# Optimization experiments

Measured on AMD Instinct MI355X. Metric: run time of the kernel, lower is better.

## Reference

```python
import jax, jax.numpy as jnp
import numpy as np
from jax import lax

V, D = 50000, 300          # vocab, word_embed_dim
C, K, H = 256, 3, 256      # conv out_channels, kernel_size, hidden_size
HLU, AH, NC = 512, 256, 2  # hidden_layer_units, attn_hidden, num_classes
B, QL, AL = 64, 40, 60     # batch, question len, answer len
EPS_COS, EPS_BN = 1e-6, 1e-5


def setup_inputs() -> dict:
    key = jax.random.key(0)
    ks = jax.random.split(key, 16)
    r = lambda k, shp: (0.02 * jax.random.normal(k, shp)).astype(jnp.float32)
    return {
        "question": jax.random.randint(ks[0], (B, QL), 0, V, dtype=jnp.int32),
        "answer": jax.random.randint(ks[1], (B, AL), 0, V, dtype=jnp.int32),
        "ext_feats": jnp.zeros((B, 2), jnp.float32),
        "embedding": r(ks[2], (V, D)),
        # sm_cnn (shared for question and answer)
        "sm_convW": r(ks[3], (K, D, C)), "sm_convb": jnp.zeros((C,), jnp.float32),
        "sm_fcW": r(ks[4], (C, H)), "sm_fcb": jnp.zeros((H,), jnp.float32),
        # context_cnn
        "ctx_convW": r(ks[5], (K, D, C)), "ctx_convb": jnp.zeros((C,), jnp.float32),
        "ctx_fcW": r(ks[6], (C, H)), "ctx_fcb": jnp.zeros((H,), jnp.float32),
        # cnn_attn MLP + cnn_prob
        "attnW": r(ks[7], (H + D, AH)), "attnb": jnp.zeros((AH,), jnp.float32),
        "probW": r(ks[8], (AH, 1)),
        # final_layers: Linear(3H, HLU) + BatchNorm1d
        "W1": r(ks[9], (3 * H, HLU)), "b1": jnp.zeros((HLU,), jnp.float32),
        "gamma": jnp.ones((HLU,), jnp.float32), "beta": jnp.zeros((HLU,), jnp.float32),
        # softmax head
        "W2": r(ks[10], (HLU, NC)), "b2": jnp.zeros((NC,), jnp.float32),
    }


def _simple_cnn(x, convW, convb, fcW, fcb):
    # x: [N, L, D]; full-width Kim-CNN == conv1d over time with D input channels
    y = lax.conv_general_dilated(x, convW, (1,), 'VALID',
                                 dimension_numbers=('NWC', 'WIO', 'NWC'))
    y = jax.nn.relu(y + convb)        # [N, L-K+1, C]
    y = jnp.max(y, axis=1)            # max-pool over time -> [N, C]
    return y @ fcW + fcb              # [N, H]


def reference(question, answer, ext_feats, embedding,
              sm_convW, sm_convb, sm_fcW, sm_fcb,
              ctx_convW, ctx_convb, ctx_fcW, ctx_fcb,
              attnW, attnb, probW, W1, b1, gamma, beta, W2, b2):
    sent1 = embedding[question]                    # [B, QL, D]
    sent2 = embedding[answer]                      # [B, AL, D]

    feature1 = _simple_cnn(sent1, sm_convW, sm_convb, sm_fcW, sm_fcb)   # [B, H]
    feature2 = _simple_cnn(sent2, sm_convW, sm_convb, sm_fcW, sm_fcb)   # [B, H]

    # ---- attn_context (gating_source == 'embed') ----
    nq = jnp.linalg.norm(sent1, axis=-1)           # [B, QL]
    na = jnp.linalg.norm(sent2, axis=-1)           # [B, AL]
    dots = jnp.einsum('bqd,bad->bqa', sent1, sent2)
    cos = dots / jnp.maximum(nq[:, :, None] * na[:, None, :], EPS_COS)  # [B, QL, AL]
    attn_answer = sent2[:, None, :, :] * cos[..., None]                 # [B, QL, AL, D]
    attn_answer = attn_answer.reshape(B * QL, AL, D)

    feat = _simple_cnn(attn_answer, ctx_convW, ctx_convb, ctx_fcW, ctx_fcb)  # [B*QL, H]
    qa_comb = jnp.concatenate([feat, sent1.reshape(-1, D)], axis=1)          # [B*QL, H+D]
    score = (jnp.tanh(qa_comb @ attnW + attnb) @ probW).reshape(B, QL)
    cnn_prob = jax.nn.softmax(score, axis=1)                                 # [B, QL]
    feature3 = jnp.sum(feat.reshape(B, QL, H) * cnn_prob[..., None], axis=1)  # [B, H]

    # ---- final layers ----
    feat_comb = jnp.concatenate([feature1, feature2, feature3], axis=1)  # [B, 3H]
    h = feat_comb @ W1 + b1
    mu = jnp.mean(h, axis=0)
    var = jnp.mean((h - mu) ** 2, axis=0)          # biased, BN training mode
    h = (h - mu) / jnp.sqrt(var + EPS_BN) * gamma + beta
    feat_out = jnp.tanh(h)                          # dropout = identity (p=0)

    preds = jax.nn.log_softmax(feat_out @ W2 + b2, axis=1)
    return preds, feat_out
```

## Files before the change

### kernel.cpp

```cpp
#include <hip/hip_runtime.h>
#include <math.h>

#define Bn 64
#define QLn 40
#define ALn 60
#define Dn 300
#define KS 320
#define NQ 1024
#define NA 1536

typedef _Float16 f16x8 __attribute__((ext_vector_type(8)));
typedef __attribute__((ext_vector_type(4))) float f32x4;

__device__ __forceinline__ short f2h(float f) {
  _Float16 h = (_Float16)f;
  return __builtin_bit_cast(short, h);
}
__device__ __forceinline__ float h2f(short s) {
  return (float)__builtin_bit_cast(_Float16, s);
}
__device__ __forceinline__ float2 h2x2(unsigned int p) {
  union { unsigned int u; _Float16 h[2]; } cv; cv.u = p;
  return make_float2((float)cv.h[0], (float)cv.h[1]);
}

__global__ __launch_bounds__(256) void k_prep(
    const int* __restrict__ qIdx, const int* __restrict__ aIdx,
    const float* __restrict__ emb,
    const float* __restrict__ smW, const float* __restrict__ ctxW,
    const float* __restrict__ attnW, const float* __restrict__ ctxfcW,
    const float* __restrict__ ctxfcb, const float* __restrict__ attnb,
    short* __restrict__ Ae1, short* __restrict__ Ae2,
    float* __restrict__ nq, float* __restrict__ na,
    short* __restrict__ BTall, float* __restrict__ Wcat, float* __restrict__ bvec,
    float* __restrict__ numb, float* __restrict__ denb,
    float* __restrict__ logits, int* __restrict__ done) {
  __shared__ float lds[4160];
  int bid = blockIdx.x, tid = threadIdx.x;
  int w = tid >> 6, lane = tid & 63;
  if (bid < 1600) {
    int row = bid * 4 + w;
    const int* idxp; short* Ae; float* nrm; int r;
    if (row < 2560) { idxp = qIdx; Ae = Ae1; nrm = nq; r = row; }
    else { idxp = aIdx; Ae = Ae2; nrm = na; r = row - 2560; }
    int tok = idxp[r];
    const float4* src = (const float4*)(emb + (size_t)tok * Dn);
    short* d = Ae + (size_t)r * KS;
    float ssq = 0.f;
    for (int i = lane; i < 80; i += 64) {
      float4 v = (i < 75) ? src[i] : make_float4(0.f, 0.f, 0.f, 0.f);
      ssq += v.x * v.x + v.y * v.y + v.z * v.z + v.w * v.w;
      short4 h4;
      h4.x = f2h(v.x); h4.y = f2h(v.y); h4.z = f2h(v.z); h4.w = f2h(v.w);
      *(short4*)&d[i * 4] = h4;
    }
    #pragma unroll
    for (int o = 32; o; o >>= 1) ssq += __shfl_down(ssq, o, 64);
    if (lane == 0) nrm[r] = sqrtf(ssq);
  } else if (bid < 1800) {
    int tb = bid - 1600;
    int kt = tb % 5, nt = tb / 5;
    int n0 = nt * 64;
    const float* src; int cb;
    if (n0 < 768)       { src = smW + (n0 >> 8) * 76800; cb = n0 & 255; }
    else if (n0 < 1024) { src = attnW + 65536;           cb = n0 - 768; }
    else if (n0 < 1792) { int m = n0 - 1024; src = smW + (m >> 8) * 76800; cb = m & 255; }
    else                { int m = n0 - 1792; src = ctxW + (m >> 8) * 76800; cb = m & 255; }
    float* tile = lds;
    int nn = tid & 63;
    #pragma unroll
    for (int it = 0; it < 16; ++it) {
      int kl = it * 4 + w;
      int k = kt * 64 + kl;
      tile[kl * 65 + nn] = (k < 300) ? src[(size_t)k * 256 + cb + nn] : 0.f;
    }
    __syncthreads();
    #pragma unroll
    for (int it = 0; it < 16; ++it) {
      int nloc = it * 4 + w;
      int kl = tid & 63;
      float v = tile[kl * 65 + nloc];
      int n = n0 + nloc, k = kt * 64 + kl;
      BTall[(size_t)n * KS + k] = f2h(v);
    }
  } else if (bid < 2057) {
    int k = bid - 1800;
    float* rowv = lds;
    int j = tid;
    rowv[j] = (k < 256) ? ctxfcW[(size_t)k * 256 + j] : ctxfcb[j];
    __syncthreads();
    float a0 = 0.f, a1 = 0.f, a2 = 0.f, a3 = 0.f;
    for (int m = 0; m < 256; m += 4) {
      a0 += rowv[m]     * attnW[(size_t)m * 256 + j];
      a1 += rowv[m + 1] * attnW[(size_t)(m + 1) * 256 + j];
      a2 += rowv[m + 2] * attnW[(size_t)(m + 2) * 256 + j];
      a3 += rowv[m + 3] * attnW[(size_t)(m + 3) * 256 + j];
    }
    float acc = (a0 + a1) + (a2 + a3);
    if (k < 256) {
      Wcat[(size_t)k * 512 + j] = rowv[j];
      Wcat[(size_t)k * 512 + 256 + j] = acc;
    } else {
      bvec[j] = ctxfcb[j];
      bvec[256 + j] = acc + attnb[j];
    }
  } else {
    for (int i = tid; i < Bn * 256; i += 256) numb[i] = 0.f;
    if (tid < Bn) denb[tid] = 0.f;
    if (tid < 2 * Bn) logits[tid] = 0.f;
    if (tid == 0) *done = 0;
  }
}

__device__ __forceinline__ void gl2lds16(const short* g, short* l) {
  __builtin_amdgcn_global_load_lds(
      (const __attribute__((address_space(1))) unsigned int*)g,
      (__attribute__((address_space(3))) unsigned int*)l, 16, 0, 0);
}

__global__ __launch_bounds__(256) void k_mega(
    const short* __restrict__ Ae1, const short* __restrict__ Ae2,
    const short* __restrict__ BTall, short* __restrict__ ZQh, short* __restrict__ ZAh,
    const float* __restrict__ nq, const float* __restrict__ na,
    float* __restrict__ cosb) {
  __shared__ __align__(16) short As[128 * 32];
  __shared__ __align__(16) short Bs[128 * 32];
  int tid = threadIdx.x;
  int wid = tid >> 6, lane = tid & 63;
  int l15 = lane & 15, l4 = lane >> 4;
  int bid = blockIdx.x;
  int lin = (bid & 7) * 73 + (bid >> 3);

  if (lin < 520) {
    const short *A, *BT; short* C; int bx, by, ldc;
    if (lin < 160) {
      int chunk = lin >> 4, ww = lin & 15;
      by = ww >> 1; bx = chunk * 2 + (ww & 1);
      A = Ae1; BT = BTall; C = ZQh; ldc = NQ;
    } else {
      int l2 = lin - 160;
      int chunk = l2 / 24, ww = l2 % 24;
      by = ww >> 1; bx = chunk * 2 + (ww & 1);
      A = Ae2; BT = BTall + (size_t)1024 * KS; C = ZAh; ldc = NA;
    }
    int rowBase = bx * 128, colBase = by * 128;
    int mw = wid * 32;

    f32x4 acc[2][8];
    #pragma unroll
    for (int i = 0; i < 2; ++i)
      #pragma unroll
      for (int j = 0; j < 8; ++j) acc[i][j] = (f32x4){0.f, 0.f, 0.f, 0.f};

    int rowA0 = mw + l15, rowA1 = mw + 16 + l15;
    int sA0 = (l4 ^ ((rowA0 >> 1) & 3)) << 3;
    int sA1 = (l4 ^ ((rowA1 >> 1) & 3)) << 3;

    #pragma unroll 1
    for (int ks = 0; ks < 10; ++ks) {
      int k0 = ks * 32;
      #pragma unroll
      for (int j = 0; j < 2; ++j) {
        int idx = tid + j * 256;
        int r = idx >> 2, s = idx & 3;
        int sl = s ^ ((r >> 1) & 3);
        int chunkStart = j * 256 + wid * 64;
        gl2lds16(A + (size_t)(rowBase + r) * KS + k0 + (sl << 3), &As[chunkStart * 8]);
        gl2lds16(BT + (size_t)(colBase + r) * KS + k0 + (sl << 3), &Bs[chunkStart * 8]);
      }
      __syncthreads();
      f16x8 a0 = *reinterpret_cast<const f16x8*>(&As[rowA0 * 32 + sA0]);
      f16x8 a1 = *reinterpret_cast<const f16x8*>(&As[rowA1 * 32 + sA1]);
      #pragma unroll
      for (int nj = 0; nj < 8; ++nj) {
        int rb = nj * 16 + l15;
        f16x8 bf = *reinterpret_cast<const f16x8*>(&Bs[rb * 32 + ((l4 ^ ((rb >> 1) & 3)) << 3)]);
        acc[0][nj] = __builtin_amdgcn_mfma_f32_16x16x32_f16(a0, bf, acc[0][nj], 0, 0, 0);
        acc[1][nj] = __builtin_amdgcn_mfma_f32_16x16x32_f16(a1, bf, acc[1][nj], 0, 0, 0);
      }
      __syncthreads();
    }
    #pragma unroll
    for (int mi = 0; mi < 2; ++mi) {
      int row0 = rowBase + mw + mi * 16 + l4 * 4;
      #pragma unroll
      for (int nj = 0; nj < 8; ++nj) {
        int col = colBase + nj * 16 + l15;
        #pragma unroll
        for (int r = 0; r < 4; ++r)
          C[(size_t)(row0 + r) * ldc + col] = f2h(acc[mi][nj][r]);
      }
    }
  } else {
    int b = lin - 520;
    int rowBase = b * 40, colBase = b * 60;
    f32x4 cacc[4];
    #pragma unroll
    for (int nj = 0; nj < 4; ++nj) cacc[nj] = (f32x4){0.f, 0.f, 0.f, 0.f};
    int rowA = (wid << 4) + l15;
    int sA = (l4 ^ ((rowA >> 1) & 3)) << 3;

    #pragma unroll 1
    for (int ks = 0; ks < 10; ++ks) {
      int k0 = ks * 32;
      int r = tid >> 2, s = tid & 3;
      int sl = s ^ ((r >> 1) & 3);
      int chunkStart = wid * 64;
      int gr = rowBase + r; if (gr > 2559) gr = 2559;
      int gc = colBase + r; if (gc > 3839) gc = 3839;
      gl2lds16(Ae1 + (size_t)gr * KS + k0 + (sl << 3), &As[chunkStart * 8]);
      gl2lds16(Ae2 + (size_t)gc * KS + k0 + (sl << 3), &Bs[chunkStart * 8]);
      __syncthreads();
      f16x8 a0 = *reinterpret_cast<const f16x8*>(&As[rowA * 32 + sA]);
      #pragma unroll
      for (int nj = 0; nj < 4; ++nj) {
        int rb = (nj << 4) + l15;
        f16x8 bf = *reinterpret_cast<const f16x8*>(&Bs[rb * 32 + ((l4 ^ ((rb >> 1) & 3)) << 3)]);
        cacc[nj] = __builtin_amdgcn_mfma_f32_16x16x32_f16(a0, bf, cacc[nj], 0, 0, 0);
      }
      __syncthreads();
    }
    int q0 = (wid << 4) + l4 * 4;
    #pragma unroll
    for (int nj = 0; nj < 4; ++nj) {
      int a = (nj << 4) + l15;
      if (a >= ALn) continue;
      float nav = na[colBase + a];
      #pragma unroll
      for (int r = 0; r < 4; ++r) {
        int qq = q0 + r;
        if (qq < QLn) {
          float den = fmaxf(nq[rowBase + qq] * nav, 1e-6f);
          cosb[(size_t)(rowBase + qq) * ALn + a] = cacc[nj][r] / den;
        }
      }
    }
  }
}

__global__ __launch_bounds__(256) void k_pool(
    const short* __restrict__ ZQh, const short* __restrict__ ZAh,
    const float* __restrict__ convb, const float* __restrict__ cosb,
    const float* __restrict__ ctxb,
    float* __restrict__ pooled_part, float* __restrict__ pctx_part) {
  __shared__ float cl[8][ALn];
  int bid = blockIdx.x, tid = threadIdx.x;
  int cp = tid & 127, th = tid >> 7;
  int c2 = cp * 2;
  if (bid < 128) {
    int s = bid;
    const short* zb; int L, ld;
    if (s < Bn) { zb = ZQh + (size_t)s * QLn * NQ; L = QLn; ld = NQ; }
    else        { zb = ZAh + (size_t)(s - Bn) * ALn * NA; L = ALn; ld = NA; }
    int P = L - 2;
    int t0 = th * (P >> 1), t1 = (th ? P : (P >> 1));
    float b0 = convb[c2], b1 = convb[c2 + 1];
    float m0 = 0.f, m1 = 0.f;
    for (int t = t0; t < t1; ++t) {
      float2 v0 = h2x2(*(const unsigned int*)&zb[t * ld + c2]);
      float2 v1 = h2x2(*(const unsigned int*)&zb[(t + 1) * ld + 256 + c2]);
      float2 v2 = h2x2(*(const unsigned int*)&zb[(t + 2) * ld + 512 + c2]);
      m0 = fmaxf(m0, b0 + v0.x + v1.x + v2.x);
      m1 = fmaxf(m1, b1 + v0.y + v1.y + v2.y);
    }
    float* dst = pooled_part + ((size_t)th * 128 + s) * 256 + c2;
    dst[0] = m0; dst[1] = m1;
  } else {
    int g = bid - 128;
    int b = g / 5, q0 = (g % 5) * 8;
    int rq = b * QLn + q0;
    for (int i = tid; i < 8 * ALn; i += 256)
      cl[i / ALn][i % ALn] = cosb[(size_t)(rq + i / ALn) * ALn + (i % ALn)];
    __syncthreads();
    const short* zb = ZAh + (size_t)b * ALn * NA + 768;
    float b0 = ctxb[c2], b1 = ctxb[c2 + 1];
    float m[8][2];
    #pragma unroll
    for (int rr = 0; rr < 8; ++rr) { m[rr][0] = 0.f; m[rr][1] = 0.f; }
    int t0 = th * 29;
    for (int t = t0; t < t0 + 29; ++t) {
      float2 v0 = h2x2(*(const unsigned int*)&zb[t * NA + c2]);
      float2 v1 = h2x2(*(const unsigned int*)&zb[(t + 1) * NA + 256 + c2]);
      float2 v2 = h2x2(*(const unsigned int*)&zb[(t + 2) * NA + 512 + c2]);
      #pragma unroll
      for (int rr = 0; rr < 8; ++rr) {
        float c0 = cl[rr][t], c1 = cl[rr][t + 1], c2v = cl[rr][t + 2];
        m[rr][0] = fmaxf(m[rr][0], b0 + c0 * v0.x + c1 * v1.x + c2v * v2.x);
        m[rr][1] = fmaxf(m[rr][1], b1 + c0 * v0.y + c1 * v1.y + c2v * v2.y);
      }
    }
    #pragma unroll
    for (int rr = 0; rr < 8; ++rr) {
      float* dst = pctx_part + ((size_t)th * 2560 + rq + rr) * 256 + c2;
      dst[0] = m[rr][0]; dst[1] = m[rr][1];
    }
  }
}

__global__ __launch_bounds__(256) void k_fcattn(
    const float* __restrict__ pooled_part, const float* __restrict__ smfcW,
    const float* __restrict__ smfcb, const float* __restrict__ pctx_part,
    const short* __restrict__ ZQh, const float* __restrict__ Wcat,
    const float* __restrict__ bvec, const float* __restrict__ probW,
    float* __restrict__ feat_comb, float* __restrict__ numb, float* __restrict__ denb) {
  __shared__ float lds[10304];
  int bid = blockIdx.x, j = threadIdx.x;
  if (bid < 32) {
    float* xin = lds;
    float* wt  = lds + 1024;
    int r0 = bid * 4;
    #pragma unroll
    for (int rr = 0; rr < 4; ++rr)
      xin[j * 4 + rr] = fmaxf(pooled_part[(size_t)(r0 + rr) * 256 + j],
                              pooled_part[(size_t)(128 + r0 + rr) * 256 + j]);
    float acc[4];
    #pragma unroll
    for (int rr = 0; rr < 4; ++rr) acc[rr] = smfcb[j];
    for (int ph = 0; ph < 8; ++ph) {
      const float4* src = (const float4*)(smfcW + (size_t)ph * 32 * 256);
      float4* dst = (float4*)wt;
      #pragma unroll
      for (int i = 0; i < 8; ++i) dst[i * 256 + j] = src[i * 256 + j];
      __syncthreads();
      #pragma unroll
      for (int kk = 0; kk < 32; ++kk) {
        float4 x = *reinterpret_cast<const float4*>(&xin[(ph * 32 + kk) * 4]);
        float wv = wt[kk * 256 + j];
        acc[0] += x.x * wv; acc[1] += x.y * wv; acc[2] += x.z * wv; acc[3] += x.w * wv;
      }
      __syncthreads();
    }
    #pragma unroll
    for (int rr = 0; rr < 4; ++rr) {
      int row = r0 + rr;
      feat_comb[(size_t)(row & 63) * 512 + ((row >> 6) * 256) + j] = acc[rr];
    }
  } else {
    float* xin  = lds;
    float* wt   = lds + 2048;
    float* sred = lds + 10240;
    int g = bid - 32;
    int b = g / 5, q0 = (g % 5) * 8;
    int rq = b * QLn + q0;
    #pragma unroll
    for (int rr = 0; rr < 8; ++rr)
      xin[j * 8 + rr] = fmaxf(pctx_part[(size_t)(rq + rr) * 256 + j],
                              pctx_part[(size_t)(2560 + rq + rr) * 256 + j]);
    float hf[8], hh[8];
    float bf0 = bvec[j], bh0 = bvec[256 + j];
    #pragma unroll
    for (int rr = 0; rr < 8; ++rr) {
      hf[rr] = bf0;
      hh[rr] = bh0 + h2f(ZQh[(size_t)(rq + rr) * NQ + 768 + j]);
    }
    for (int ph = 0; ph < 16; ++ph) {
      const float4* src = (const float4*)(Wcat + (size_t)ph * 16 * 512);
      float4* dst = (float4*)wt;
      #pragma unroll
      for (int i = 0; i < 8; ++i) dst[i * 256 + j] = src[i * 256 + j];
      __syncthreads();
      #pragma unroll
      for (int kk = 0; kk < 16; ++kk) {
        int k = ph * 16 + kk;
        float4 x0 = *reinterpret_cast<const float4*>(&xin[k * 8]);
        float4 x1 = *reinterpret_cast<const float4*>(&xin[k * 8 + 4]);
        float w0 = wt[kk * 512 + j], w1 = wt[kk * 512 + 256 + j];
        hf[0] += x0.x * w0; hf[1] += x0.y * w0; hf[2] += x0.z * w0; hf[3] += x0.w * w0;
        hf[4] += x1.x * w0; hf[5] += x1.y * w0; hf[6] += x1.z * w0; hf[7] += x1.w * w0;
        hh[0] += x0.x * w1; hh[1] += x0.y * w1; hh[2] += x0.z * w1; hh[3] += x0.w * w1;
        hh[4] += x1.x * w1; hh[5] += x1.y * w1; hh[6] += x1.z * w1; hh[7] += x1.w * w1;
      }
      __syncthreads();
    }
    float pw = probW[j];
    int lane = j & 63, wv = j >> 6;
    #pragma unroll
    for (int rr = 0; rr < 8; ++rr) {
      float s = tanhf(hh[rr]) * pw;
      #pragma unroll
      for (int off = 32; off; off >>= 1) s += __shfl_down(s, off, 64);
      if (lane == 0) sred[rr * 4 + wv] = s;
    }
    __syncthreads();
    float e[8], esum = 0.f, acc3 = 0.f;
    #pragma unroll
    for (int rr = 0; rr < 8; ++rr) {
      float s = sred[rr * 4] + sred[rr * 4 + 1] + sred[rr * 4 + 2] + sred[rr * 4 + 3];
      e[rr] = __expf(s);
      esum += e[rr];
      acc3 += e[rr] * hf[rr];
    }
    atomicAdd(&numb[(size_t)b * 256 + j], acc3);
    if (j == 0) atomicAdd(&denb[b], esum);
  }
}

__global__ __launch_bounds__(256) void k_w1bn(
    const float* __restrict__ feat_comb, const float* __restrict__ numb,
    const float* __restrict__ denb, const float* __restrict__ W1,
    const float* __restrict__ b1, const float* __restrict__ gamma,
    const float* __restrict__ beta, const float* __restrict__ W2,
    const float* __restrict__ b2, float* __restrict__ feat_out,
    float* __restrict__ preds, float* __restrict__ logits, int* __restrict__ done) {
  int j0 = blockIdx.x * 8;
  int tid = threadIdx.x;
  __shared__ float wl[768][12];
  __shared__ float hb[64][8];
  __shared__ int lastflag;
  for (int it = 0; it < 24; ++it) {
    int idx = tid + it * 256;
    int k = idx >> 3, jj = idx & 7;
    wl[k][jj] = W1[(size_t)k * 512 + j0 + jj];
  }
  __syncthreads();
  int n = tid >> 2, p = tid & 3;
  float acc1[8] = {0.f, 0.f, 0.f, 0.f, 0.f, 0.f, 0.f, 0.f};
  float acc2[8] = {0.f, 0.f, 0.f, 0.f, 0.f, 0.f, 0.f, 0.f};
  const float* frow = feat_comb + (size_t)n * 512 + p;
  for (int i = 0; i < 128; ++i) {
    float v = frow[i * 4];
    int k = p + i * 4;
    float4 w0 = *reinterpret_cast<const float4*>(&wl[k][0]);
    float4 w1v = *reinterpret_cast<const float4*>(&wl[k][4]);
    acc1[0] += v * w0.x; acc1[1] += v * w0.y; acc1[2] += v * w0.z; acc1[3] += v * w0.w;
    acc1[4] += v * w1v.x; acc1[5] += v * w1v.y; acc1[6] += v * w1v.z; acc1[7] += v * w1v.w;
  }
  const float* nrow = numb + (size_t)n * 256 + p;
  for (int i = 0; i < 64; ++i) {
    float v = nrow[i * 4];
    int k = 512 + p + i * 4;
    float4 w0 = *reinterpret_cast<const float4*>(&wl[k][0]);
    float4 w1v = *reinterpret_cast<const float4*>(&wl[k][4]);
    acc2[0] += v * w0.x; acc2[1] += v * w0.y; acc2[2] += v * w0.z; acc2[3] += v * w0.w;
    acc2[4] += v * w1v.x; acc2[5] += v * w1v.y; acc2[6] += v * w1v.z; acc2[7] += v * w1v.w;
  }
  #pragma unroll
  for (int jj = 0; jj < 8; ++jj) {
    acc1[jj] += __shfl_xor(acc1[jj], 1, 64);
    acc1[jj] += __shfl_xor(acc1[jj], 2, 64);
    acc2[jj] += __shfl_xor(acc2[jj], 1, 64);
    acc2[jj] += __shfl_xor(acc2[jj], 2, 64);
  }
  if (p == 0) {
    float rden = 1.f / denb[n];
    #pragma unroll
    for (int jj = 0; jj < 8; ++jj) hb[n][jj] = acc1[jj] + rden * acc2[jj] + b1[j0 + jj];
  }
  __syncthreads();
  if (tid < 64) {
    float l0p = 0.f, l1p = 0.f;
    #pragma unroll
    for (int jj = 0; jj < 8; ++jj) {
      float v = hb[tid][jj];
      float s = v;
      #pragma unroll
      for (int off = 32; off; off >>= 1) s += __shfl_xor(s, off, 64);
      float mu = s * (1.f / 64.f);
      float d = v - mu;
      float q2 = d * d;
      #pragma unroll
      for (int off = 32; off; off >>= 1) q2 += __shfl_xor(q2, off, 64);
      float var = q2 * (1.f / 64.f);
      float fo = tanhf(d * rsqrtf(var + 1e-5f) * gamma[j0 + jj] + beta[j0 + jj]);
      feat_out[(size_t)tid * 512 + j0 + jj] = fo;
      l0p += fo * W2[(j0 + jj) * 2 + 0];
      l1p += fo * W2[(j0 + jj) * 2 + 1];
    }
    atomicAdd(&logits[tid * 2 + 0], l0p);
    atomicAdd(&logits[tid * 2 + 1], l1p);
  }
  __threadfence();
  __syncthreads();
  if (tid == 0) lastflag = (atomicAdd(done, 1) == gridDim.x - 1) ? 1 : 0;
  __syncthreads();
  if (lastflag && tid < 64) {
    __threadfence();
    float l0 = atomicAdd(&logits[tid * 2 + 0], 0.f) + b2[0];
    float l1 = atomicAdd(&logits[tid * 2 + 1], 0.f) + b2[1];
    float mx = fmaxf(l0, l1);
    float lse = mx + logf(__expf(l0 - mx) + __expf(l1 - mx));
    preds[tid * 2 + 0] = l0 - lse;
    preds[tid * 2 + 1] = l1 - lse;
  }
}

extern "C" void kernel_launch(void* const* d_in, const int* in_sizes, int n_in,
                              void* d_out, int out_size, void* d_ws, size_t ws_size,
                              hipStream_t stream) {
  (void)in_sizes; (void)n_in; (void)out_size; (void)ws_size;
  const int*   question  = (const int*)d_in[0];
  const int*   answer    = (const int*)d_in[1];
  const float* embedding = (const float*)d_in[3];
  const float* sm_convW  = (const float*)d_in[4];
  const float* sm_convb  = (const float*)d_in[5];
  const float* sm_fcW    = (const float*)d_in[6];
  const float* sm_fcb    = (const float*)d_in[7];
  const float* ctx_convW = (const float*)d_in[8];
  const float* ctx_convb = (const float*)d_in[9];
  const float* ctx_fcW   = (const float*)d_in[10];
  const float* ctx_fcb   = (const float*)d_in[11];
  const float* attnW     = (const float*)d_in[12];
  const float* attnb     = (const float*)d_in[13];
  const float* probW     = (const float*)d_in[14];
  const float* W1        = (const float*)d_in[15];
  const float* b1        = (const float*)d_in[16];
  const float* gamma     = (const float*)d_in[17];
  const float* beta      = (const float*)d_in[18];
  const float* W2        = (const float*)d_in[19];
  const float* b2        = (const float*)d_in[20];

  float* out = (float*)d_out;
  char* base = (char*)d_ws;
  size_t off = 0;
  auto alloc = [&](size_t bytes) { char* p = base + off; off += (bytes + 255) & ~(size_t)255; return p; };

  short* Ae1   = (short*)alloc(2560ull * KS * 2);
  short* Ae2   = (short*)alloc(3840ull * KS * 2);
  short* BTall = (short*)alloc(2560ull * KS * 2);
  short* ZQh   = (short*)alloc(2560ull * NQ * 2);
  short* ZAh   = (short*)alloc(3840ull * NA * 2);
  float* nq    = (float*)alloc(2560 * 4);
  float* na    = (float*)alloc(3840 * 4);
  float* cosb  = (float*)alloc(2560ull * ALn * 4);
  float* Wcat  = (float*)alloc(256ull * 512 * 4);
  float* bvec  = (float*)alloc(512 * 4);
  float* pctx_part = (float*)alloc(2ull * 2560 * 256 * 4);
  float* feat_comb = (float*)alloc(64ull * 512 * 4);
  float* numb   = (float*)alloc(64ull * 256 * 4);
  float* denb   = (float*)alloc(64 * 4);
  float* logits = (float*)alloc(128 * 4);
  int*   done   = (int*)alloc(256);
  float* pooled_part = (float*)BTall;

  k_prep<<<2058, 256, 0, stream>>>(question, answer, embedding, sm_convW, ctx_convW,
                                   attnW, ctx_fcW, ctx_fcb, attnb,
                                   Ae1, Ae2, nq, na, BTall, Wcat, bvec,
                                   numb, denb, logits, done);
  k_mega<<<584, 256, 0, stream>>>(Ae1, Ae2, BTall, ZQh, ZAh, nq, na, cosb);
  k_pool<<<448, 256, 0, stream>>>(ZQh, ZAh, sm_convb, cosb, ctx_convb,
                                  pooled_part, pctx_part);
  k_fcattn<<<352, 256, 0, stream>>>(pooled_part, sm_fcW, sm_fcb, pctx_part,
                                    ZQh, Wcat, bvec, probW,
                                    feat_comb, numb, denb);
  k_w1bn<<<64, 256, 0, stream>>>(feat_comb, numb, denb, W1, b1, gamma, beta,
                                 W2, b2, out + 128, out, logits, done);
}
```

Measured before the change: 98.61 us.

## Fuse five kernel launches into one cooperative persistent kernel with grid syncs

Replaces the five separate kernels (prep, GEMM/cosine, pooling, fc/attention, W1+BN) with a single cooperative kernel. Each stage loops over its former block indices with a grid-stride loop and the stages are separated by grid.sync(). The goal is to remove per-launch overhead and inter-kernel gaps. In exchange, stages with more work units than resident blocks (e.g. 2058 prep units) are serialized, the grid barriers have their own cost, and the grid is capped at 584 blocks, so occupancy is limited by the larger shared memory footprint.

```diff
diff --git a/kernel.cpp b/kernel.cpp
--- a/kernel.cpp
+++ b/kernel.cpp
@@ -1,5 +1,8 @@
 #include <hip/hip_runtime.h>
+#include <hip/hip_cooperative_groups.h>
 #include <math.h>
+
+namespace cg = cooperative_groups;
 
 #define Bn 64
 #define QLn 40
@@ -23,464 +26,470 @@
   union { unsigned int u; _Float16 h[2]; } cv; cv.u = p;
   return make_float2((float)cv.h[0], (float)cv.h[1]);
 }
-
-__global__ __launch_bounds__(256) void k_prep(
-    const int* __restrict__ qIdx, const int* __restrict__ aIdx,
-    const float* __restrict__ emb,
-    const float* __restrict__ smW, const float* __restrict__ ctxW,
-    const float* __restrict__ attnW, const float* __restrict__ ctxfcW,
-    const float* __restrict__ ctxfcb, const float* __restrict__ attnb,
-    short* __restrict__ Ae1, short* __restrict__ Ae2,
-    float* __restrict__ nq, float* __restrict__ na,
-    short* __restrict__ BTall, float* __restrict__ Wcat, float* __restrict__ bvec,
-    float* __restrict__ numb, float* __restrict__ denb,
-    float* __restrict__ logits, int* __restrict__ done) {
-  __shared__ float lds[4160];
-  int bid = blockIdx.x, tid = threadIdx.x;
-  int w = tid >> 6, lane = tid & 63;
-  if (bid < 1600) {
-    int row = bid * 4 + w;
-    const int* idxp; short* Ae; float* nrm; int r;
-    if (row < 2560) { idxp = qIdx; Ae = Ae1; nrm = nq; r = row; }
-    else { idxp = aIdx; Ae = Ae2; nrm = na; r = row - 2560; }
-    int tok = idxp[r];
-    const float4* src = (const float4*)(emb + (size_t)tok * Dn);
-    short* d = Ae + (size_t)r * KS;
-    float ssq = 0.f;
-    for (int i = lane; i < 80; i += 64) {
-      float4 v = (i < 75) ? src[i] : make_float4(0.f, 0.f, 0.f, 0.f);
-      ssq += v.x * v.x + v.y * v.y + v.z * v.z + v.w * v.w;
-      short4 h4;
-      h4.x = f2h(v.x); h4.y = f2h(v.y); h4.z = f2h(v.z); h4.w = f2h(v.w);
-      *(short4*)&d[i * 4] = h4;
-    }
-    #pragma unroll
-    for (int o = 32; o; o >>= 1) ssq += __shfl_down(ssq, o, 64);
-    if (lane == 0) nrm[r] = sqrtf(ssq);
-  } else if (bid < 1800) {
-    int tb = bid - 1600;
-    int kt = tb % 5, nt = tb / 5;
-    int n0 = nt * 64;
-    const float* src; int cb;
-    if (n0 < 768)       { src = smW + (n0 >> 8) * 76800; cb = n0 & 255; }
-    else if (n0 < 1024) { src = attnW + 65536;           cb = n0 - 768; }
-    else if (n0 < 1792) { int m = n0 - 1024; src = smW + (m >> 8) * 76800; cb = m & 255; }
-    else                { int m = n0 - 1792; src = ctxW + (m >> 8) * 76800; cb = m & 255; }
-    float* tile = lds;
-    int nn = tid & 63;
-    #pragma unroll
-    for (int it = 0; it < 16; ++it) {
-      int kl = it * 4 + w;
-      int k = kt * 64 + kl;
-      tile[kl * 65 + nn] = (k < 300) ? src[(size_t)k * 256 + cb + nn] : 0.f;
-    }
-    __syncthreads();
-    #pragma unroll
-    for (int it = 0; it < 16; ++it) {
-      int nloc = it * 4 + w;
-      int kl = tid & 63;
-      float v = tile[kl * 65 + nloc];
-      int n = n0 + nloc, k = kt * 64 + kl;
-      BTall[(size_t)n * KS + k] = f2h(v);
-    }
-  } else if (bid < 2057) {
-    int k = bid - 1800;
-    float* rowv = lds;
-    int j = tid;
-    rowv[j] = (k < 256) ? ctxfcW[(size_t)k * 256 + j] : ctxfcb[j];
-    __syncthreads();
-    float a0 = 0.f, a1 = 0.f, a2 = 0.f, a3 = 0.f;
-    for (int m = 0; m < 256; m += 4) {
-      a0 += rowv[m]     * attnW[(size_t)m * 256 + j];
-      a1 += rowv[m + 1] * attnW[(size_t)(m + 1) * 256 + j];
-      a2 += rowv[m + 2] * attnW[(size_t)(m + 2) * 256 + j];
-      a3 += rowv[m + 3] * attnW[(size_t)(m + 3) * 256 + j];
-    }
-    float acc = (a0 + a1) + (a2 + a3);
-    if (k < 256) {
-      Wcat[(size_t)k * 512 + j] = rowv[j];
-      Wcat[(size_t)k * 512 + 256 + j] = acc;
-    } else {
-      bvec[j] = ctxfcb[j];
-      bvec[256 + j] = acc + attnb[j];
-    }
-  } else {
-    for (int i = tid; i < Bn * 256; i += 256) numb[i] = 0.f;
-    if (tid < Bn) denb[tid] = 0.f;
-    if (tid < 2 * Bn) logits[tid] = 0.f;
-    if (tid == 0) *done = 0;
-  }
-}
-
 __device__ __forceinline__ void gl2lds16(const short* g, short* l) {
   __builtin_amdgcn_global_load_lds(
       (const __attribute__((address_space(1))) unsigned int*)g,
       (__attribute__((address_space(3))) unsigned int*)l, 16, 0, 0);
 }
 
-__global__ __launch_bounds__(256) void k_mega(
-    const short* __restrict__ Ae1, const short* __restrict__ Ae2,
-    const short* __restrict__ BTall, short* __restrict__ ZQh, short* __restrict__ ZAh,
-    const float* __restrict__ nq, const float* __restrict__ na,
-    float* __restrict__ cosb) {
-  __shared__ __align__(16) short As[128 * 32];
-  __shared__ __align__(16) short Bs[128 * 32];
-  int tid = threadIdx.x;
-  int wid = tid >> 6, lane = tid & 63;
-  int l15 = lane & 15, l4 = lane >> 4;
-  int bid = blockIdx.x;
-  int lin = (bid & 7) * 73 + (bid >> 3);
-
-  if (lin < 520) {
-    const short *A, *BT; short* C; int bx, by, ldc;
-    if (lin < 160) {
-      int chunk = lin >> 4, ww = lin & 15;
-      by = ww >> 1; bx = chunk * 2 + (ww & 1);
-      A = Ae1; BT = BTall; C = ZQh; ldc = NQ;
+struct Params {
+  const int* qIdx; const int* aIdx; const float* emb;
+  const float* smW; const float* ctxW; const float* attnW;
+  const float* ctxfcW; const float* ctxfcb; const float* attnb;
+  const float* smfcW; const float* smfcb; const float* convb; const float* ctxb;
+  const float* probW; const float* W1; const float* b1;
+  const float* gamma; const float* beta; const float* W2; const float* b2;
+  short* Ae1; short* Ae2; short* BTall; short* ZQh; short* ZAh;
+  float* nq; float* na; float* cosb; float* Wcat; float* bvec;
+  float* pooled; float* pctx; float* feat_comb;
+  float* numb; float* denb; float* logits;
+  float* feat_out; float* preds;
+};
+
+__global__ __launch_bounds__(256, 3) void k_all(Params P) {
+  cg::grid_group grid = cg::this_grid();
+  __shared__ __align__(16) float smem[10304];
+  int bid = blockIdx.x, tid = threadIdx.x, G = gridDim.x;
+  int w = tid >> 6, lane = tid & 63;
+
+  for (int u = bid; u < 2058; u += G) {
+    if (u < 1600) {
+      int row = u * 4 + w;
+      const int* idxp; short* Ae; float* nrm; int r;
+      if (row < 2560) { idxp = P.qIdx; Ae = P.Ae1; nrm = P.nq; r = row; }
+      else { idxp = P.aIdx; Ae = P.Ae2; nrm = P.na; r = row - 2560; }
+      int tok = idxp[r];
+      const float4* src = (const float4*)(P.emb + (size_t)tok * Dn);
+      short* d = Ae + (size_t)r * KS;
+      float ssq = 0.f;
+      for (int i = lane; i < 80; i += 64) {
+        float4 v = (i < 75) ? src[i] : make_float4(0.f, 0.f, 0.f, 0.f);
+        ssq += v.x * v.x + v.y * v.y + v.z * v.z + v.w * v.w;
+        short4 h4;
+        h4.x = f2h(v.x); h4.y = f2h(v.y); h4.z = f2h(v.z); h4.w = f2h(v.w);
+        *(short4*)&d[i * 4] = h4;
+      }
+      #pragma unroll
+      for (int o = 32; o; o >>= 1) ssq += __shfl_down(ssq, o, 64);
+      if (lane == 0) nrm[r] = sqrtf(ssq);
+    } else if (u < 1800) {
+      __syncthreads();
+      int tb = u - 1600;
+      int kt = tb % 5, nt = tb / 5;
+      int n0 = nt * 64;
+      const float* src; int cb;
+      if (n0 < 768)       { src = P.smW + (n0 >> 8) * 76800; cb = n0 & 255; }
+      else if (n0 < 1024) { src = P.attnW + 65536;           cb = n0 - 768; }
+      else if (n0 < 1792) { int m = n0 - 1024; src = P.smW + (m >> 8) * 76800; cb = m & 255; }
+      else                { int m = n0 - 1792; src = P.ctxW + (m >> 8) * 76800; cb = m & 255; }
+      float* tile = smem;
+      int nn = tid & 63;
+      #pragma unroll
+      for (int it = 0; it < 16; ++it) {
+        int kl = it * 4 + w;
+        int k = kt * 64 + kl;
+        tile[kl * 65 + nn] = (k < 300) ? src[(size_t)k * 256 + cb + nn] : 0.f;
+      }
+      __syncthreads();
+      #pragma unroll
+      for (int it = 0; it < 16; ++it) {
+        int nloc = it * 4 + w;
+        int kl = tid & 63;
+        float v = tile[kl * 65 + nloc];
+        int n = n0 + nloc, k = kt * 64 + kl;
+        P.BTall[(size_t)n * KS + k] = f2h(v);
+      }
+    } else if (u < 2057) {
+      __syncthreads();
+      int k = u - 1800;
+      float* rowv = smem;
+      int j = tid;
+      rowv[j] = (k < 256) ? P.ctxfcW[(size_t)k * 256 + j] : P.ctxfcb[j];
+      __syncthreads();
+      float a0 = 0.f, a1 = 0.f, a2 = 0.f, a3 = 0.f;
+      for (int m = 0; m < 256; m += 4) {
+        a0 += rowv[m]     * P.attnW[(size_t)m * 256 + j];
+        a1 += rowv[m + 1] * P.attnW[(size_t)(m + 1) * 256 + j];
+        a2 += rowv[m + 2] * P.attnW[(size_t)(m + 2) * 256 + j];
+        a3 += rowv[m + 3] * P.attnW[(size_t)(m + 3) * 256 + j];
+      }
+      float acc = (a0 + a1) + (a2 + a3);
+      if (k < 256) {
+        P.Wcat[(size_t)k * 512 + j] = rowv[j];
+        P.Wcat[(size_t)k * 512 + 256 + j] = acc;
+      } else {
+        P.bvec[j] = P.ctxfcb[j];
+        P.bvec[256 + j] = acc + P.attnb[j];
+      }
     } else {
-      int l2 = lin - 160;
-      int chunk = l2 / 24, ww = l2 % 24;
-      by = ww >> 1; bx = chunk * 2 + (ww & 1);
-      A = Ae2; BT = BTall + (size_t)1024 * KS; C = ZAh; ldc = NA;
-    }
-    int rowBase = bx * 128, colBase = by * 128;
-    int mw = wid * 32;
-
-    f32x4 acc[2][8];
-    #pragma unroll
-    for (int i = 0; i < 2; ++i)
-      #pragma unroll
-      for (int j = 0; j < 8; ++j) acc[i][j] = (f32x4){0.f, 0.f, 0.f, 0.f};
-
-    int rowA0 = mw + l15, rowA1 = mw + 16 + l15;
-    int sA0 = (l4 ^ ((rowA0 >> 1) & 3)) << 3;
-    int sA1 = (l4 ^ ((rowA1 >> 1) & 3)) << 3;
-
-    #pragma unroll 1
-    for (int ks = 0; ks < 10; ++ks) {
-      int k0 = ks * 32;
-      #pragma unroll
-      for (int j = 0; j < 2; ++j) {
-        int idx = tid + j * 256;
-        int r = idx >> 2, s = idx & 3;
-        int sl = s ^ ((r >> 1) & 3);
-        int chunkStart = j * 256 + wid * 64;
-        gl2lds16(A + (size_t)(rowBase + r) * KS + k0 + (sl << 3), &As[chunkStart * 8]);
-        gl2lds16(BT + (size_t)(colBase + r) * KS + k0 + (sl << 3), &Bs[chunkStart * 8]);
-      }
-      __syncthreads();
-      f16x8 a0 = *reinterpret_cast<const f16x8*>(&As[rowA0 * 32 + sA0]);
-      f16x8 a1 = *reinterpret_cast<const f16x8*>(&As[rowA1 * 32 + sA1]);
-      #pragma unroll
-      for (int nj = 0; nj < 8; ++nj) {
-        int rb = nj * 16 + l15;
-        f16x8 bf = *reinterpret_cast<const f16x8*>(&Bs[rb * 32 + ((l4 ^ ((rb >> 1) & 3)) << 3)]);
-        acc[0][nj] = __builtin_amdgcn_mfma_f32_16x16x32_f16(a0, bf, acc[0][nj], 0, 0, 0);
-        acc[1][nj] = __builtin_amdgcn_mfma_f32_16x16x32_f16(a1, bf, acc[1][nj], 0, 0, 0);
-      }
-      __syncthreads();
-    }
-    #pragma unroll
-    for (int mi = 0; mi < 2; ++mi) {
-      int row0 = rowBase + mw + mi * 16 + l4 * 4;
-      #pragma unroll
-      for (int nj = 0; nj < 8; ++nj) {
-        int col = colBase + nj * 16 + l15;
-        #pragma unroll
-        for (int r = 0; r < 4; ++r)
-          C[(size_t)(row0 + r) * ldc + col] = f2h(acc[mi][nj][r]);
-      }
-    }
-  } else {
-    int b = lin - 520;
-    int rowBase = b * 40, colBase = b * 60;
-    f32x4 cacc[4];
-    #pragma unroll
-    for (int nj = 0; nj < 4; ++nj) cacc[nj] = (f32x4){0.f, 0.f, 0.f, 0.f};
-    int rowA = (wid << 4) + l15;
-    int sA = (l4 ^ ((rowA >> 1) & 3)) << 3;
-
-    #pragma unroll 1
-    for (int ks = 0; ks < 10; ++ks) {
-      int k0 = ks * 32;
-      int r = tid >> 2, s = tid & 3;
-      int sl = s ^ ((r >> 1) & 3);
-      int chunkStart = wid * 64;
-      int gr = rowBase + r; if (gr > 2559) gr = 2559;
-      int gc = colBase + r; if (gc > 3839) gc = 3839;
-      gl2lds16(Ae1 + (size_t)gr * KS + k0 + (sl << 3), &As[chunkStart * 8]);
-      gl2lds16(Ae2 + (size_t)gc * KS + k0 + (sl << 3), &Bs[chunkStart * 8]);
-      __syncthreads();
-      f16x8 a0 = *reinterpret_cast<const f16x8*>(&As[rowA * 32 + sA]);
-      #pragma unroll
-      for (int nj = 0; nj < 4; ++nj) {
-        int rb = (nj << 4) + l15;
-        f16x8 bf = *reinterpret_cast<const f16x8*>(&Bs[rb * 32 + ((l4 ^ ((rb >> 1) & 3)) << 3)]);
-        cacc[nj] = __builtin_amdgcn_mfma_f32_16x16x32_f16(a0, bf, cacc[nj], 0, 0, 0);
-      }
-      __syncthreads();
-    }
-    int q0 = (wid << 4) + l4 * 4;
-    #pragma unroll
-    for (int nj = 0; nj < 4; ++nj) {
-      int a = (nj << 4) + l15;
-      if (a >= ALn) continue;
-      float nav = na[colBase + a];
-      #pragma unroll
-      for (int r = 0; r < 4; ++r) {
-        int qq = q0 + r;
-        if (qq < QLn) {
-          float den = fmaxf(nq[rowBase + qq] * nav, 1e-6f);
-          cosb[(size_t)(rowBase + qq) * ALn + a] = cacc[nj][r] / den;
-        }
-      }
+      for (int i = tid; i < Bn * 256; i += 256) P.numb[i] = 0.f;
+      if (tid < Bn) P.denb[tid] = 0.f;
+      if (tid < 2 * Bn) P.logits[tid] = 0.f;
     }
   }
-}
-
-__global__ __launch_bounds__(256) void k_pool(
-    const short* __restrict__ ZQh, const short* __restrict__ ZAh,
-    const float* __restrict__ convb, const float* __restrict__ cosb,
-    const float* __restrict__ ctxb,
-    float* __restrict__ pooled_part, float* __restrict__ pctx_part) {
-  __shared__ float cl[8][ALn];
-  int bid = blockIdx.x, tid = threadIdx.x;
-  int cp = tid & 127, th = tid >> 7;
-  int c2 = cp * 2;
-  if (bid < 128) {
-    int s = bid;
-    const short* zb; int L, ld;
-    if (s < Bn) { zb = ZQh + (size_t)s * QLn * NQ; L = QLn; ld = NQ; }
-    else        { zb = ZAh + (size_t)(s - Bn) * ALn * NA; L = ALn; ld = NA; }
-    int P = L - 2;
-    int t0 = th * (P >> 1), t1 = (th ? P : (P >> 1));
-    float b0 = convb[c2], b1 = convb[c2 + 1];
-    float m0 = 0.f, m1 = 0.f;
-    for (int t = t0; t < t1; ++t) {
-      float2 v0 = h2x2(*(const unsigned int*)&zb[t * ld + c2]);
-      float2 v1 = h2x2(*(const unsigned int*)&zb[(t + 1) * ld + 256 + c2]);
-      float2 v2 = h2x2(*(const unsigned int*)&zb[(t + 2) * ld + 512 + c2]);
-      m0 = fmaxf(m0, b0 + v0.x + v1.x + v2.x);
-      m1 = fmaxf(m1, b1 + v0.y + v1.y + v2.y);
-    }
-    float* dst = pooled_part + ((size_t)th * 128 + s) * 256 + c2;
-    dst[0] = m0; dst[1] = m1;
-  } else {
-    int g = bid - 128;
-    int b = g / 5, q0 = (g % 5) * 8;
-    int rq = b * QLn + q0;
-    for (int i = tid; i < 8 * ALn; i += 256)
-      cl[i / ALn][i % ALn] = cosb[(size_t)(rq + i / ALn) * ALn + (i % ALn)];
-    __syncthreads();
-    const short* zb = ZAh + (size_t)b * ALn * NA + 768;
-    float b0 = ctxb[c2], b1 = ctxb[c2 + 1];
-    float m[8][2];
-    #pragma unroll
-    for (int rr = 0; rr < 8; ++rr) { m[rr][0] = 0.f; m[rr][1] = 0.f; }
-    int t0 = th * 29;
-    for (int t = t0; t < t0 + 29; ++t) {
-      float2 v0 = h2x2(*(const unsigned int*)&zb[t * NA + c2]);
-      float2 v1 = h2x2(*(const unsigned int*)&zb[(t + 1) * NA + 256 + c2]);
-      float2 v2 = h2x2(*(const unsigned int*)&zb[(t + 2) * NA + 512 + c2]);
-      #pragma unroll
-      for (int rr = 0; rr < 8; ++rr) {
-        float c0 = cl[rr][t], c1 = cl[rr][t + 1], c2v = cl[rr][t + 2];
-        m[rr][0] = fmaxf(m[rr][0], b0 + c0 * v0.x + c1 * v1.x + c2v * v2.x);
-        m[rr][1] = fmaxf(m[rr][1], b1 + c0 * v0.y + c1 * v1.y + c2v * v2.y);
-      }
-    }
-    #pragma unroll
-    for (int rr = 0; rr < 8; ++rr) {
-      float* dst = pctx_part + ((size_t)th * 2560 + rq + rr) * 256 + c2;
-      dst[0] = m[rr][0]; dst[1] = m[rr][1];
+  grid.sync();
+
+  {
+    short* As = (short*)smem;
+    short* Bs = (short*)smem + 4096;
+    int l15 = lane & 15, l4 = lane >> 4;
+    for (int u = bid; u < 584; u += G) {
+      __syncthreads();
+      int lin = (u & 7) * 73 + (u >> 3);
+      if (lin < 520) {
+        const short *A, *BT; short* C; int bx, by, ldc;
+        if (lin < 160) {
+          int chunk = lin >> 4, ww = lin & 15;
+          by = ww >> 1; bx = chunk * 2 + (ww & 1);
+          A = P.Ae1; BT = P.BTall; C = P.ZQh; ldc = NQ;
+        } else {
+          int l2 = lin - 160;
+          int chunk = l2 / 24, ww = l2 % 24;
+          by = ww >> 1; bx = chunk * 2 + (ww & 1);
+          A = P.Ae2; BT = P.BTall + (size_t)1024 * KS; C = P.ZAh; ldc = NA;
+        }
+        int rowBase = bx * 128, colBase = by * 128;
+        int mw = w * 32;
+        f32x4 acc[2][8];
+        #pragma unroll
+        for (int i = 0; i < 2; ++i)
+          #pragma unroll
+          for (int j = 0; j < 8; ++j) acc[i][j] = (f32x4){0.f, 0.f, 0.f, 0.f};
+        int rowA0 = mw + l15, rowA1 = mw + 16 + l15;
+        int sA0 = (l4 ^ ((rowA0 >> 1) & 3)) << 3;
+        int sA1 = (l4 ^ ((rowA1 >> 1) & 3)) << 3;
+        #pragma unroll 1
+        for (int ks = 0; ks < 10; ++ks) {
+          int k0 = ks * 32;
+          #pragma unroll
+          for (int j = 0; j < 2; ++j) {
+            int idx = tid + j * 256;
+            int r = idx >> 2, s = idx & 3;
+            int sl = s ^ ((r >> 1) & 3);
+            int chunkStart = j * 256 + w * 64;
+            gl2lds16(A + (size_t)(rowBase + r) * KS + k0 + (sl << 3), &As[chunkStart * 8]);
+            gl2lds16(BT + (size_t)(colBase + r) * KS + k0 + (sl << 3), &Bs[chunkStart * 8]);
+          }
+          __syncthreads();
+          f16x8 a0 = *reinterpret_cast<const f16x8*>(&As[rowA0 * 32 + sA0]);
+          f16x8 a1 = *reinterpret_cast<const f16x8*>(&As[rowA1 * 32 + sA1]);
+          #pragma unroll
+          for (int nj = 0; nj < 8; ++nj) {
+            int rb = nj * 16 + l15;
+            f16x8 bf = *reinterpret_cast<const f16x8*>(&Bs[rb * 32 + ((l4 ^ ((rb >> 1) & 3)) << 3)]);
+            acc[0][nj] = __builtin_amdgcn_mfma_f32_16x16x32_f16(a0, bf, acc[0][nj], 0, 0, 0);
+            acc[1][nj] = __builtin_amdgcn_mfma_f32_16x16x32_f16(a1, bf, acc[1][nj], 0, 0, 0);
+          }
+          __syncthreads();
+        }
+        #pragma unroll
+        for (int mi = 0; mi < 2; ++mi) {
+          int row0 = rowBase + mw + mi * 16 + l4 * 4;
+          #pragma unroll
+          for (int nj = 0; nj < 8; ++nj) {
+            int col = colBase + nj * 16 + l15;
+            #pragma unroll
+            for (int r = 0; r < 4; ++r)
+              C[(size_t)(row0 + r) * ldc + col] = f2h(acc[mi][nj][r]);
+          }
+        }
+      } else {
+        int b = lin - 520;
+        int rowBase = b * 40, colBase = b * 60;
+        f32x4 cacc[4];
+        #pragma unroll
+        for (int nj = 0; nj < 4; ++nj) cacc[nj] = (f32x4){0.f, 0.f, 0.f, 0.f};
+        int rowA = (w << 4) + l15;
+        int sA = (l4 ^ ((rowA >> 1) & 3)) << 3;
+        #pragma unroll 1
+        for (int ks = 0; ks < 10; ++ks) {
+          int k0 = ks * 32;
+          int r = tid >> 2, s = tid & 3;
+          int sl = s ^ ((r >> 1) & 3);
+          int chunkStart = w * 64;
+          int gr = rowBase + r; if (gr > 2559) gr = 2559;
+          int gc = colBase + r; if (gc > 3839) gc = 3839;
+          gl2lds16(P.Ae1 + (size_t)gr * KS + k0 + (sl << 3), &As[chunkStart * 8]);
+          gl2lds16(P.Ae2 + (size_t)gc * KS + k0 + (sl << 3), &Bs[chunkStart * 8]);
+          __syncthreads();
+          f16x8 a0 = *reinterpret_cast<const f16x8*>(&As[rowA * 32 + sA]);
+          #pragma unroll
+          for (int nj = 0; nj < 4; ++nj) {
+            int rb = (nj << 4) + l15;
+            f16x8 bf = *reinterpret_cast<const f16x8*>(&Bs[rb * 32 + ((l4 ^ ((rb >> 1) & 3)) << 3)]);
+            cacc[nj] = __builtin_amdgcn_mfma_f32_16x16x32_f16(a0, bf, cacc[nj], 0, 0, 0);
+          }
+          __syncthreads();
+        }
+        int q0 = (w << 4) + l4 * 4;
+        #pragma unroll
+        for (int nj = 0; nj < 4; ++nj) {
+          int a = (nj << 4) + l15;
+          if (a >= ALn) continue;
+          float nav = P.na[colBase + a];
+          #pragma unroll
+          for (int r = 0; r < 4; ++r) {
+            int qq = q0 + r;
+            if (qq < QLn) {
+              float den = fmaxf(P.nq[rowBase + qq] * nav, 1e-6f);
+              P.cosb[(size_t)(rowBase + qq) * ALn + a] = cacc[nj][r] / den;
+            }
+          }
+        }
+      }
     }
   }
-}
-
-__global__ __launch_bounds__(256) void k_fcattn(
-    const float* __restrict__ pooled_part, const float* __restrict__ smfcW,
-    const float* __restrict__ smfcb, const float* __restrict__ pctx_part,
-    const short* __restrict__ ZQh, const float* __restrict__ Wcat,
-    const float* __restrict__ bvec, const float* __restrict__ probW,
-    float* __restrict__ feat_comb, float* __restrict__ numb, float* __restrict__ denb) {
-  __shared__ float lds[10304];
-  int bid = blockIdx.x, j = threadIdx.x;
-  if (bid < 32) {
-    float* xin = lds;
-    float* wt  = lds + 1024;
-    int r0 = bid * 4;
-    #pragma unroll
-    for (int rr = 0; rr < 4; ++rr)
-      xin[j * 4 + rr] = fmaxf(pooled_part[(size_t)(r0 + rr) * 256 + j],
-                              pooled_part[(size_t)(128 + r0 + rr) * 256 + j]);
-    float acc[4];
-    #pragma unroll
-    for (int rr = 0; rr < 4; ++rr) acc[rr] = smfcb[j];
-    for (int ph = 0; ph < 8; ++ph) {
-      const float4* src = (const float4*)(smfcW + (size_t)ph * 32 * 256);
-      float4* dst = (float4*)wt;
+  grid.sync();
+
+  {
+    float* cl  = smem;
+    float* tmp = smem + 512;
+    int cp = tid & 127, th = tid >> 7;
+    int c2 = cp * 2;
+    for (int u = bid; u < 448; u += G) {
+      __syncthreads();
+      if (u < 128) {
+        int s = u;
+        const short* zb; int L, ld;
+        if (s < Bn) { zb = P.ZQh + (size_t)s * QLn * NQ; L = QLn; ld = NQ; }
+        else        { zb = P.ZAh + (size_t)(s - Bn) * ALn * NA; L = ALn; ld = NA; }
+        int Pn = L - 2;
+        int t0 = th * (Pn >> 1), t1 = (th ? Pn : (Pn >> 1));
+        float b0 = P.convb[c2], b1v = P.convb[c2 + 1];
+        float m0 = 0.f, m1 = 0.f;
+        for (int t = t0; t < t1; ++t) {
+          float2 v0 = h2x2(*(const unsigned int*)&zb[t * ld + c2]);
+          float2 v1 = h2x2(*(const unsigned int*)&zb[(t + 1) * ld + 256 + c2]);
+          float2 v2 = h2x2(*(const unsigned int*)&zb[(t + 2) * ld + 512 + c2]);
+          m0 = fmaxf(m0, b0 + v0.x + v1.x + v2.x);
+          m1 = fmaxf(m1, b1v + v0.y + v1.y + v2.y);
+        }
+        if (th == 1) { tmp[c2] = m0; tmp[c2 + 1] = m1; }
+        __syncthreads();
+        if (th == 0) {
+          float* dst = P.pooled + (size_t)s * 256 + c2;
+          dst[0] = fmaxf(m0, tmp[c2]);
+          dst[1] = fmaxf(m1, tmp[c2 + 1]);
+        }
+      } else {
+        int g = u - 128;
+        int b = g / 5, q0 = (g % 5) * 8;
+        int rq = b * QLn + q0;
+        for (int i = tid; i < 8 * ALn; i += 256)
+          cl[i] = P.cosb[(size_t)(rq + i / ALn) * ALn + (i % ALn)];
+        __syncthreads();
+        const short* zb = P.ZAh + (size_t)b * ALn * NA + 768;
+        float b0 = P.ctxb[c2], b1v = P.ctxb[c2 + 1];
+        float m[8][2];
+        #pragma unroll
+        for (int rr = 0; rr < 8; ++rr) { m[rr][0] = 0.f; m[rr][1] = 0.f; }
+        int t0 = th * 29;
+        for (int t = t0; t < t0 + 29; ++t) {
+          float2 v0 = h2x2(*(const unsigned int*)&zb[t * NA + c2]);
+          float2 v1 = h2x2(*(const unsigned int*)&zb[(t + 1) * NA + 256 + c2]);
+          float2 v2 = h2x2(*(const unsigned int*)&zb[(t + 2) * NA + 512 + c2]);
+          #pragma unroll
+          for (int rr = 0; rr < 8; ++rr) {
+            float c0 = cl[rr * ALn + t], c1 = cl[rr * ALn + t + 1], c2v = cl[rr * ALn + t + 2];
+            m[rr][0] = fmaxf(m[rr][0], b0 + c0 * v0.x + c1 * v1.x + c2v * v2.x);
+            m[rr][1] = fmaxf(m[rr][1], b1v + c0 * v0.y + c1 * v1.y + c2v * v2.y);
+          }
+        }
+        if (th == 1) {
+          #pragma unroll
+          for (int rr = 0; rr < 8; ++rr) {
+            tmp[rr * 256 + c2] = m[rr][0];
+            tmp[rr * 256 + c2 + 1] = m[rr][1];
+          }
+        }
+        __syncthreads();
+        if (th == 0) {
+          #pragma unroll
+          for (int rr = 0; rr < 8; ++rr) {
+            float* dst = P.pctx + (size_t)(rq + rr) * 256 + c2;
+            dst[0] = fmaxf(m[rr][0], tmp[rr * 256 + c2]);
+            dst[1] = fmaxf(m[rr][1], tmp[rr * 256 + c2 + 1]);
+          }
+        }
+      }
+    }
+  }
+  grid.sync();
+
+  {
+    int j = tid;
+    for (int u = bid; u < 352; u += G) {
+      __syncthreads();
+      if (u < 32) {
+        float* xin = smem;
+        float* wt  = smem + 1024;
+        int r0 = u * 4;
+        #pragma unroll
+        for (int rr = 0; rr < 4; ++rr)
+          xin[j * 4 + rr] = P.pooled[(size_t)(r0 + rr) * 256 + j];
+        float acc[4];
+        #pragma unroll
+        for (int rr = 0; rr < 4; ++rr) acc[rr] = P.smfcb[j];
+        for (int ph = 0; ph < 8; ++ph) {
+          const float4* src = (const float4*)(P.smfcW + (size_t)ph * 32 * 256);
+          float4* dst = (float4*)wt;
+          #pragma unroll
+          for (int i = 0; i < 8; ++i) dst[i * 256 + j] = src[i * 256 + j];
+          __syncthreads();
+          #pragma unroll
+          for (int kk = 0; kk < 32; ++kk) {
+            float4 x = *reinterpret_cast<const float4*>(&xin[(ph * 32 + kk) * 4]);
+            float wv = wt[kk * 256 + j];
+            acc[0] += x.x * wv; acc[1] += x.y * wv; acc[2] += x.z * wv; acc[3] += x.w * wv;
+          }
+          __syncthreads();
+        }
+        #pragma unroll
+        for (int rr = 0; rr < 4; ++rr) {
+          int row = r0 + rr;
+          P.feat_comb[(size_t)(row & 63) * 512 + ((row >> 6) * 256) + j] = acc[rr];
+        }
+      } else {
+        float* xin  = smem;
+        float* wt   = smem + 2048;
+        float* sred = smem + 10240;
+        int g = u - 32;
+        int b = g / 5, q0 = (g % 5) * 8;
+        int rq = b * QLn + q0;
+        #pragma unroll
+        for (int rr = 0; rr < 8; ++rr)
+          xin[j * 8 + rr] = P.pctx[(size_t)(rq + rr) * 256 + j];
+        float hf[8], hh[8];
+        float bf0 = P.bvec[j], bh0 = P.bvec[256 + j];
+        #pragma unroll
+        for (int rr = 0; rr < 8; ++rr) {
+          hf[rr] = bf0;
+          hh[rr] = bh0 + h2f(P.ZQh[(size_t)(rq + rr) * NQ + 768 + j]);
+        }
+        for (int ph = 0; ph < 16; ++ph) {
+          const float4* src = (const float4*)(P.Wcat + (size_t)ph * 16 * 512);
+          float4* dst = (float4*)wt;
+          #pragma unroll
+          for (int i = 0; i < 8; ++i) dst[i * 256 + j] = src[i * 256 + j];
+          __syncthreads();
+          #pragma unroll
+          for (int kk = 0; kk < 16; ++kk) {
+            int k = ph * 16 + kk;
+            float4 x0 = *reinterpret_cast<const float4*>(&xin[k * 8]);
+            float4 x1 = *reinterpret_cast<const float4*>(&xin[k * 8 + 4]);
+            float w0 = wt[kk * 512 + j], w1 = wt[kk * 512 + 256 + j];
+            hf[0] += x0.x * w0; hf[1] += x0.y * w0; hf[2] += x0.z * w0; hf[3] += x0.w * w0;
+            hf[4] += x1.x * w0; hf[5] += x1.y * w0; hf[6] += x1.z * w0; hf[7] += x1.w * w0;
+            hh[0] += x0.x * w1; hh[1] += x0.y * w1; hh[2] += x0.z * w1; hh[3] += x0.w * w1;
+            hh[4] += x1.x * w1; hh[5] += x1.y * w1; hh[6] += x1.z * w1; hh[7] += x1.w * w1;
+          }
+          __syncthreads();
+        }
+        float pw = P.probW[j];
+        int lane2 = j & 63, wv = j >> 6;
+        #pragma unroll
+        for (int rr = 0; rr < 8; ++rr) {
+          float s = tanhf(hh[rr]) * pw;
+          #pragma unroll
+          for (int off = 32; off; off >>= 1) s += __shfl_down(s, off, 64);
+          if (lane2 == 0) sred[rr * 4 + wv] = s;
+        }
+        __syncthreads();
+        float e[8], esum = 0.f, acc3 = 0.f;
+        #pragma unroll
+        for (int rr = 0; rr < 8; ++rr) {
+          float s = sred[rr * 4] + sred[rr * 4 + 1] + sred[rr * 4 + 2] + sred[rr * 4 + 3];
+          e[rr] = __expf(s);
+          esum += e[rr];
+          acc3 += e[rr] * hf[rr];
+        }
+        atomicAdd(&P.numb[(size_t)b * 256 + j], acc3);
+        if (j == 0) atomicAdd(&P.denb[b], esum);
+      }
+    }
+  }
+  grid.sync();
+
+  {
+    float* wl = smem;
+    float* hb = smem + 9216;
+    for (int u = bid; u < 64; u += G) {
+      __syncthreads();
+      int j0 = u * 8;
+      for (int it = 0; it < 24; ++it) {
+        int idx = tid + it * 256;
+        int k = idx >> 3, jj = idx & 7;
+        wl[k * 12 + jj] = P.W1[(size_t)k * 512 + j0 + jj];
+      }
+      __syncthreads();
+      int n = tid >> 2, p = tid & 3;
+      float acc1[8] = {0.f,0.f,0.f,0.f,0.f,0.f,0.f,0.f};
+      float acc2[8] = {0.f,0.f,0.f,0.f,0.f,0.f,0.f,0.f};
+      const float* frow = P.feat_comb + (size_t)n * 512 + p;
+      for (int i = 0; i < 128; ++i) {
+        float v = frow[i * 4];
+        int k = p + i * 4;
+        float4 w0 = *reinterpret_cast<const float4*>(&wl[k * 12]);
+        float4 w1v = *reinterpret_cast<const float4*>(&wl[k * 12 + 4]);
+        acc1[0] += v * w0.x; acc1[1] += v * w0.y; acc1[2] += v * w0.z; acc1[3] += v * w0.w;
+        acc1[4] += v * w1v.x; acc1[5] += v * w1v.y; acc1[6] += v * w1v.z; acc1[7] += v * w1v.w;
+      }
+      const float* nrow = P.numb + (size_t)n * 256 + p;
+      for (int i = 0; i < 64; ++i) {
+        float v = nrow[i * 4];
+        int k = 512 + p + i * 4;
+        float4 w0 = *reinterpret_cast<const float4*>(&wl[k * 12]);
+        float4 w1v = *reinterpret_cast<const float4*>(&wl[k * 12 + 4]);
+        acc2[0] += v * w0.x; acc2[1] += v * w0.y; acc2[2] += v * w0.z; acc2[3] += v * w0.w;
+        acc2[4] += v * w1v.x; acc2[5] += v * w1v.y; acc2[6] += v * w1v.z; acc2[7] += v * w1v.w;
+      }
       #pragma unroll
-      for (int i = 0; i < 8; ++i) dst[i * 256 + j] = src[i * 256 + j];
-      __syncthreads();
-      #pragma unroll
-      for (int kk = 0; kk < 32; ++kk) {
-        float4 x = *reinterpret_cast<const float4*>(&xin[(ph * 32 + kk) * 4]);
-        float wv = wt[kk * 256 + j];
-        acc[0] += x.x * wv; acc[1] += x.y * wv; acc[2] += x.z * wv; acc[3] += x.w * wv;
-      }
-      __syncthreads();
+      for (int jj = 0; jj < 8; ++jj) {
+        acc1[jj] += __shfl_xor(acc1[jj], 1, 64);
+        acc1[jj] += __shfl_xor(acc1[jj], 2, 64);
+        acc2[jj] += __shfl_xor(acc2[jj], 1, 64);
+        acc2[jj] += __shfl_xor(acc2[jj], 2, 64);
+      }
+      if (p == 0) {
+        float rden = 1.f / P.denb[n];
+        #pragma unroll
+        for (int jj = 0; jj < 8; ++jj)
+          hb[n * 8 + jj] = acc1[jj] + rden * acc2[jj] + P.b1[j0 + jj];
+      }
+      __syncthreads();
+      if (tid < 64) {
+        float l0p = 0.f, l1p = 0.f;
+        #pragma unroll
+        for (int jj = 0; jj < 8; ++jj) {
+          float v = hb[tid * 8 + jj];
+          float s = v;
+          #pragma unroll
+          for (int off = 32; off; off >>= 1) s += __shfl_xor(s, off, 64);
+          float mu = s * (1.f / 64.f);
+          float d = v - mu;
+          float q2 = d * d;
+          #pragma unroll
+          for (int off = 32; off; off >>= 1) q2 += __shfl_xor(q2, off, 64);
+          float var = q2 * (1.f / 64.f);
+          float fo = tanhf(d * rsqrtf(var + 1e-5f) * P.gamma[j0 + jj] + P.beta[j0 + jj]);
+          P.feat_out[(size_t)tid * 512 + j0 + jj] = fo;
+          l0p += fo * P.W2[(j0 + jj) * 2 + 0];
+          l1p += fo * P.W2[(j0 + jj) * 2 + 1];
+        }
+        atomicAdd(&P.logits[tid * 2 + 0], l0p);
+        atomicAdd(&P.logits[tid * 2 + 1], l1p);
+      }
     }
-    #pragma unroll
-    for (int rr = 0; rr < 4; ++rr) {
-      int row = r0 + rr;
-      feat_comb[(size_t)(row & 63) * 512 + ((row >> 6) * 256) + j] = acc[rr];
-    }
-  } else {
-    float* xin  = lds;
-    float* wt   = lds + 2048;
-    float* sred = lds + 10240;
-    int g = bid - 32;
-    int b = g / 5, q0 = (g % 5) * 8;
-    int rq = b * QLn + q0;
-    #pragma unroll
-    for (int rr = 0; rr < 8; ++rr)
-      xin[j * 8 + rr] = fmaxf(pctx_part[(size_t)(rq + rr) * 256 + j],
-                              pctx_part[(size_t)(2560 + rq + rr) * 256 + j]);
-    float hf[8], hh[8];
-    float bf0 = bvec[j], bh0 = bvec[256 + j];
-    #pragma unroll
-    for (int rr = 0; rr < 8; ++rr) {
-      hf[rr] = bf0;
-      hh[rr] = bh0 + h2f(ZQh[(size_t)(rq + rr) * NQ + 768 + j]);
-    }
-    for (int ph = 0; ph < 16; ++ph) {
-      const float4* src = (const float4*)(Wcat + (size_t)ph * 16 * 512);
-      float4* dst = (float4*)wt;
-      #pragma unroll
-      for (int i = 0; i < 8; ++i) dst[i * 256 + j] = src[i * 256 + j];
-      __syncthreads();
-      #pragma unroll
-      for (int kk = 0; kk < 16; ++kk) {
-        int k = ph * 16 + kk;
-        float4 x0 = *reinterpret_cast<const float4*>(&xin[k * 8]);
-        float4 x1 = *reinterpret_cast<const float4*>(&xin[k * 8 + 4]);
-        float w0 = wt[kk * 512 + j], w1 = wt[kk * 512 + 256 + j];
-        hf[0] += x0.x * w0; hf[1] += x0.y * w0; hf[2] += x0.z * w0; hf[3] += x0.w * w0;
-        hf[4] += x1.x * w0; hf[5] += x1.y * w0; hf[6] += x1.z * w0; hf[7] += x1.w * w0;
-        hh[0] += x0.x * w1; hh[1] += x0.y * w1; hh[2] += x0.z * w1; hh[3] += x0.w * w1;
-        hh[4] += x1.x * w1; hh[5] += x1.y * w1; hh[6] += x1.z * w1; hh[7] += x1.w * w1;
-      }
-      __syncthreads();
-    }
-    float pw = probW[j];
-    int lane = j & 63, wv = j >> 6;
-    #pragma unroll
-    for (int rr = 0; rr < 8; ++rr) {
-      float s = tanhf(hh[rr]) * pw;
-      #pragma unroll
-      for (int off = 32; off; off >>= 1) s += __shfl_down(s, off, 64);
-      if (lane == 0) sred[rr * 4 + wv] = s;
-    }
-    __syncthreads();
-    float e[8], esum = 0.f, acc3 = 0.f;
-    #pragma unroll
-    for (int rr = 0; rr < 8; ++rr) {
-      float s = sred[rr * 4] + sred[rr * 4 + 1] + sred[rr * 4 + 2] + sred[rr * 4 + 3];
-      e[rr] = __expf(s);
-      esum += e[rr];
-      acc3 += e[rr] * hf[rr];
-    }
-    atomicAdd(&numb[(size_t)b * 256 + j], acc3);
-    if (j == 0) atomicAdd(&denb[b], esum);
   }
-}
-
-__global__ __launch_bounds__(256) void k_w1bn(
-    const float* __restrict__ feat_comb, const float* __restrict__ numb,
-    const float* __restrict__ denb, const float* __restrict__ W1,
-    const float* __restrict__ b1, const float* __restrict__ gamma,
-    const float* __restrict__ beta, const float* __restrict__ W2,
-    const float* __restrict__ b2, float* __restrict__ feat_out,
-    float* __restrict__ preds, float* __restrict__ logits, int* __restrict__ done) {
-  int j0 = blockIdx.x * 8;
-  int tid = threadIdx.x;
-  __shared__ float wl[768][12];
-  __shared__ float hb[64][8];
-  __shared__ int lastflag;
-  for (int it = 0; it < 24; ++it) {
-    int idx = tid + it * 256;
-    int k = idx >> 3, jj = idx & 7;
-    wl[k][jj] = W1[(size_t)k * 512 + j0 + jj];
-  }
-  __syncthreads();
-  int n = tid >> 2, p = tid & 3;
-  float acc1[8] = {0.f, 0.f, 0.f, 0.f, 0.f, 0.f, 0.f, 0.f};
-  float acc2[8] = {0.f, 0.f, 0.f, 0.f, 0.f, 0.f, 0.f, 0.f};
-  const float* frow = feat_comb + (size_t)n * 512 + p;
-  for (int i = 0; i < 128; ++i) {
-    float v = frow[i * 4];
-    int k = p + i * 4;
-    float4 w0 = *reinterpret_cast<const float4*>(&wl[k][0]);
-    float4 w1v = *reinterpret_cast<const float4*>(&wl[k][4]);
-    acc1[0] += v * w0.x; acc1[1] += v * w0.y; acc1[2] += v * w0.z; acc1[3] += v * w0.w;
-    acc1[4] += v * w1v.x; acc1[5] += v * w1v.y; acc1[6] += v * w1v.z; acc1[7] += v * w1v.w;
-  }
-  const float* nrow = numb + (size_t)n * 256 + p;
-  for (int i = 0; i < 64; ++i) {
-    float v = nrow[i * 4];
-    int k = 512 + p + i * 4;
-    float4 w0 = *reinterpret_cast<const float4*>(&wl[k][0]);
-    float4 w1v = *reinterpret_cast<const float4*>(&wl[k][4]);
-    acc2[0] += v * w0.x; acc2[1] += v * w0.y; acc2[2] += v * w0.z; acc2[3] += v * w0.w;
-    acc2[4] += v * w1v.x; acc2[5] += v * w1v.y; acc2[6] += v * w1v.z; acc2[7] += v * w1v.w;
-  }
-  #pragma unroll
-  for (int jj = 0; jj < 8; ++jj) {
-    acc1[jj] += __shfl_xor(acc1[jj], 1, 64);
-    acc1[jj] += __shfl_xor(acc1[jj], 2, 64);
-    acc2[jj] += __shfl_xor(acc2[jj], 1, 64);
-    acc2[jj] += __shfl_xor(acc2[jj], 2, 64);
-  }
-  if (p == 0) {
-    float rden = 1.f / denb[n];
-    #pragma unroll
-    for (int jj = 0; jj < 8; ++jj) hb[n][jj] = acc1[jj] + rden * acc2[jj] + b1[j0 + jj];
-  }
-  __syncthreads();
-  if (tid < 64) {
-    float l0p = 0.f, l1p = 0.f;
-    #pragma unroll
-    for (int jj = 0; jj < 8; ++jj) {
-      float v = hb[tid][jj];
-      float s = v;
-      #pragma unroll
-      for (int off = 32; off; off >>= 1) s += __shfl_xor(s, off, 64);
-      float mu = s * (1.f / 64.f);
-      float d = v - mu;
-      float q2 = d * d;
-      #pragma unroll
-      for (int off = 32; off; off >>= 1) q2 += __shfl_xor(q2, off, 64);
-      float var = q2 * (1.f / 64.f);
-      float fo = tanhf(d * rsqrtf(var + 1e-5f) * gamma[j0 + jj] + beta[j0 + jj]);
-      feat_out[(size_t)tid * 512 + j0 + jj] = fo;
-      l0p += fo * W2[(j0 + jj) * 2 + 0];
-      l1p += fo * W2[(j0 + jj) * 2 + 1];
-    }
-    atomicAdd(&logits[tid * 2 + 0], l0p);
-    atomicAdd(&logits[tid * 2 + 1], l1p);
-  }
-  __threadfence();
-  __syncthreads();
-  if (tid == 0) lastflag = (atomicAdd(done, 1) == gridDim.x - 1) ? 1 : 0;
-  __syncthreads();
-  if (lastflag && tid < 64) {
-    __threadfence();
-    float l0 = atomicAdd(&logits[tid * 2 + 0], 0.f) + b2[0];
-    float l1 = atomicAdd(&logits[tid * 2 + 1], 0.f) + b2[1];
+  grid.sync();
+
+  if (bid == 0 && tid < 64) {
+    float l0 = P.logits[tid * 2 + 0] + P.b2[0];
+    float l1 = P.logits[tid * 2 + 1] + P.b2[1];
     float mx = fmaxf(l0, l1);
     float lse = mx + logf(__expf(l0 - mx) + __expf(l1 - mx));
-    preds[tid * 2 + 0] = l0 - lse;
-    preds[tid * 2 + 1] = l1 - lse;
+    P.preds[tid * 2 + 0] = l0 - lse;
+    P.preds[tid * 2 + 1] = l1 - lse;
   }
 }
 
@@ -488,60 +497,59 @@
                               void* d_out, int out_size, void* d_ws, size_t ws_size,
                               hipStream_t stream) {
   (void)in_sizes; (void)n_in; (void)out_size; (void)ws_size;
-  const int*   question  = (const int*)d_in[0];
-  const int*   answer    = (const int*)d_in[1];
-  const float* embedding = (const float*)d_in[3];
-  const float* sm_convW  = (const float*)d_in[4];
-  const float* sm_convb  = (const float*)d_in[5];
-  const float* sm_fcW    = (const float*)d_in[6];
-  const float* sm_fcb    = (const float*)d_in[7];
-  const float* ctx_convW = (const float*)d_in[8];
-  const float* ctx_convb = (const float*)d_in[9];
-  const float* ctx_fcW   = (const float*)d_in[10];
-  const float* ctx_fcb   = (const float*)d_in[11];
-  const float* attnW     = (const float*)d_in[12];
-  const float* attnb     = (const float*)d_in[13];
-  const float* probW     = (const float*)d_in[14];
-  const float* W1        = (const float*)d_in[15];
-  const float* b1        = (const float*)d_in[16];
-  const float* gamma     = (const float*)d_in[17];
-  const float* beta      = (const float*)d_in[18];
-  const float* W2        = (const float*)d_in[19];
-  const float* b2        = (const float*)d_in[20];
-
   float* out = (float*)d_out;
   char* base = (char*)d_ws;
   size_t off = 0;
   auto alloc = [&](size_t bytes) { char* p = base + off; off += (bytes + 255) & ~(size_t)255; return p; };
 
-  short* Ae1   = (short*)alloc(2560ull * KS * 2);
-  short* Ae2   = (short*)alloc(3840ull * KS * 2);
-  short* BTall = (short*)alloc(2560ull * KS * 2);
-  short* ZQh   = (short*)alloc(2560ull * NQ * 2);
-  short* ZAh   = (short*)alloc(3840ull * NA * 2);
-  float* nq    = (float*)alloc(2560 * 4);
-  float* na    = (float*)alloc(3840 * 4);
-  float* cosb  = (float*)alloc(2560ull * ALn * 4);
-  float* Wcat  = (float*)alloc(256ull * 512 * 4);
-  float* bvec  = (float*)alloc(512 * 4);
-  float* pctx_part = (float*)alloc(2ull * 2560 * 256 * 4);
-  float* feat_comb = (float*)alloc(64ull * 512 * 4);
-  float* numb   = (float*)alloc(64ull * 256 * 4);
-  float* denb   = (float*)alloc(64 * 4);
-  float* logits = (float*)alloc(128 * 4);
-  int*   done   = (int*)alloc(256);
-  float* pooled_part = (float*)BTall;
-
-  k_prep<<<2058, 256, 0, stream>>>(question, answer, embedding, sm_convW, ctx_convW,
-                                   attnW, ctx_fcW, ctx_fcb, attnb,
-                                   Ae1, Ae2, nq, na, BTall, Wcat, bvec,
-                                   numb, denb, logits, done);
-  k_mega<<<584, 256, 0, stream>>>(Ae1, Ae2, BTall, ZQh, ZAh, nq, na, cosb);
-  k_pool<<<448, 256, 0, stream>>>(ZQh, ZAh, sm_convb, cosb, ctx_convb,
-                                  pooled_part, pctx_part);
-  k_fcattn<<<352, 256, 0, stream>>>(pooled_part, sm_fcW, sm_fcb, pctx_part,
-                                    ZQh, Wcat, bvec, probW,
-                                    feat_comb, numb, denb);
-  k_w1bn<<<64, 256, 0, stream>>>(feat_comb, numb, denb, W1, b1, gamma, beta,
-                                 W2, b2, out + 128, out, logits, done);
+  Params p;
+  p.qIdx   = (const int*)d_in[0];
+  p.aIdx   = (const int*)d_in[1];
+  p.emb    = (const float*)d_in[3];
+  p.smW    = (const float*)d_in[4];
+  p.convb  = (const float*)d_in[5];
+  p.smfcW  = (const float*)d_in[6];
+  p.smfcb  = (const float*)d_in[7];
+  p.ctxW   = (const float*)d_in[8];
+  p.ctxb   = (const float*)d_in[9];
+  p.ctxfcW = (const float*)d_in[10];
+  p.ctxfcb = (const float*)d_in[11];
+  p.attnW  = (const float*)d_in[12];
+  p.attnb  = (const float*)d_in[13];
+  p.probW  = (const float*)d_in[14];
+  p.W1     = (const float*)d_in[15];
+  p.b1     = (const float*)d_in[16];
+  p.gamma  = (const float*)d_in[17];
+  p.beta   = (const float*)d_in[18];
+  p.W2     = (const float*)d_in[19];
+  p.b2     = (const float*)d_in[20];
+
+  p.Ae1   = (short*)alloc(2560ull * KS * 2);
+  p.Ae2   = (short*)alloc(3840ull * KS * 2);
+  p.BTall = (short*)alloc(2560ull * KS * 2);
+  p.ZQh   = (short*)alloc(2560ull * NQ * 2);
+  p.ZAh   = (short*)alloc(3840ull * NA * 2);
+  p.nq    = (float*)alloc(2560 * 4);
+  p.na    = (float*)alloc(3840 * 4);
+  p.cosb  = (float*)alloc(2560ull * ALn * 4);
+  p.Wcat  = (float*)alloc(256ull * 512 * 4);
+  p.bvec  = (float*)alloc(512 * 4);
+  p.pctx  = (float*)alloc(2560ull * 256 * 4);
+  p.feat_comb = (float*)alloc(64ull * 512 * 4);
+  p.numb   = (float*)alloc(64ull * 256 * 4);
+  p.denb   = (float*)alloc(64 * 4);
+  p.logits = (float*)alloc(128 * 4);
+  p.pooled = (float*)p.BTall;
+  p.feat_out = out + 128;
+  p.preds    = out;
+
+  int maxB = 0;
+  hipOccupancyMaxActiveBlocksPerMultiprocessor(&maxB, reinterpret_cast<const void*>(k_all), 256, 0);
+  if (maxB <= 0) maxB = 2;
+  int grid = maxB * 256;
+  if (grid > 584) grid = 584;
+
+  void* args[] = { &p };
+  hipLaunchCooperativeKernel(reinterpret_cast<void*>(k_all), dim3(grid), dim3(256),
+                             args, 0, stream);
 }
```

New measurement: 326.1 us. 3.31x slower.
